# Performance work log

Measured on AMD Instinct MI355X. Metric: run time of the kernel, lower is better.

Reference implementation:

```python
import jax, jax.numpy as jnp
import numpy as np

N, E, G = 20000, 640000, 64
D_IN, H, C, D_OUT = 256, 4, 64, 32
HC = H * C


def gat_layer(x, W, a_src, a_dst, b, src, dst, n_nodes, heads, ch):
    # x: [N, F_in], W: [F_in, H*C]
    h = (x @ W).reshape(n_nodes, heads, ch)          # [N,H,C]
    es = jnp.einsum('nhc,hc->nh', h, a_src)          # [N,H]
    ed = jnp.einsum('nhc,hc->nh', h, a_dst)
    e = jax.nn.leaky_relu(es[src] + ed[dst], 0.2)    # [Etot,H]
    m = jax.ops.segment_max(e, dst, num_segments=n_nodes)
    m = jnp.where(jnp.isfinite(m), m, 0.0)
    ex = jnp.exp(e - m[dst])
    denom = jax.ops.segment_sum(ex, dst, num_segments=n_nodes)
    alpha = ex / jnp.maximum(denom[dst], 1e-16)      # softmax over in-edges per dst
    out = jax.ops.segment_sum(alpha[:, :, None] * h[src], dst, num_segments=n_nodes)
    return out.reshape(n_nodes, heads * ch) + b


def setup_inputs() -> dict:
    key = jax.random.key(0)
    ks = jax.random.split(key, 14)
    g1 = 1.0 / np.sqrt(D_IN)
    g2 = 1.0 / np.sqrt(HC)
    inp = {
        'x': jax.random.normal(ks[0], (N, D_IN), jnp.float32),
        'edge_index': jax.random.randint(ks[1], (2, E), 0, N, jnp.int64 if jax.config.jax_enable_x64 else jnp.int32),
        'batch': jnp.sort(jax.random.randint(ks[2], (N,), 0, G)),
        'W1': jax.random.normal(ks[3], (D_IN, HC), jnp.float32) * g1,
        'a_src1': jax.random.normal(ks[4], (H, C), jnp.float32) * g2,
        'a_dst1': jax.random.normal(ks[5], (H, C), jnp.float32) * g2,
        'b1': jnp.zeros((HC,), jnp.float32),
        'W2': jax.random.normal(ks[6], (HC, HC), jnp.float32) * g2,
        'a_src2': jax.random.normal(ks[7], (H, C), jnp.float32) * g2,
        'a_dst2': jax.random.normal(ks[8], (H, C), jnp.float32) * g2,
        'b2': jnp.zeros((HC,), jnp.float32),
        'Wp': jax.random.normal(ks[9], (HC, D_OUT), jnp.float32) * g2,
        'bp': jnp.zeros((D_OUT,), jnp.float32),
    }
    return inp


def reference(x, edge_index, batch, W1, a_src1, a_dst1, b1, W2, a_src2, a_dst2, b2, Wp, bp):
    # add self-loops (PyG GATConv default)
    loop = jnp.arange(N, dtype=edge_index.dtype)
    src = jnp.concatenate([edge_index[0], loop])
    dst = jnp.concatenate([edge_index[1], loop])
    x1 = jax.nn.relu(gat_layer(x, W1, a_src1, a_dst1, b1, src, dst, N, H, C))
    # dropout p=0.6 is identity in eval mode
    x2 = jax.nn.relu(gat_layer(x1, W2, a_src2, a_dst2, b2, src, dst, N, H, C))
    node_scores = x2 @ Wp + bp                        # [N, D_OUT]
    sums = jax.ops.segment_sum(node_scores, batch, num_segments=G)
    counts = jax.ops.segment_sum(jnp.ones((N,), node_scores.dtype), batch, num_segments=G)
    return sums / jnp.maximum(counts, 1.0)[:, None]   # [G, D_OUT]
```

## Files before the change

### kernel.cpp

```cpp
#include <hip/hip_runtime.h>
#include <hip/hip_bf16.h>
#include <cstdint>

#define NNODES 20000
#define NEDGES 640000
#define ETOT   (NEDGES + NNODES)
#define NGROUP 64
#define HC     256
#define DOUT   32

typedef short bf16x8 __attribute__((ext_vector_type(8)));
typedef short s16x4  __attribute__((ext_vector_type(4)));
typedef float f32x4  __attribute__((ext_vector_type(4)));
typedef float f32x2  __attribute__((ext_vector_type(2)));
typedef int   s32x4  __attribute__((ext_vector_type(4)));
typedef unsigned int u32x4 __attribute__((ext_vector_type(4)));

__device__ __forceinline__ float b2f(__hip_bfloat16 v) { return __bfloat162float(v); }
__device__ __forceinline__ float bs2f(short v) {
    union { unsigned int u; float f; } c; c.u = ((unsigned int)(unsigned short)v) << 16; return c.f;
}
__device__ __forceinline__ short f2bs(float v) {
    __hip_bfloat16 b = __float2bfloat16(v);
    union { __hip_bfloat16 b; short s; } u; u.b = b; return u.s;
}
__device__ __forceinline__ float ldf(const void* __restrict__ p, size_t i, int bf) {
    return bf ? __bfloat162float(((const __hip_bfloat16*)p)[i]) : ((const float*)p)[i];
}
__device__ __forceinline__ int ld_idx(const int* __restrict__ p, size_t i, int f64) {
    return f64 ? p[2 * i] : p[i];
}

__global__ void k_probe(const unsigned int* __restrict__ xw, const int* __restrict__ ei,
                        int* __restrict__ flag, int* __restrict__ deg) {
    int t = blockIdx.x * 256 + threadIdx.x;
    for (int i = t; i < NNODES; i += 256 * 32) deg[i] = 0;
    if (blockIdx.x == 0 && threadIdx.x < 64) {
        int l = threadIdx.x;
        int ones = 0, zeros = 0;
#pragma unroll
        for (int r = 0; r < 4; r++) {
            unsigned long long b1 = __ballot((xw[r * 64 + l] >> 14) & 1);
            unsigned long long b2 = __ballot(ei[2 * (r * 64 + l) + 1] == 0);
            ones  += __popcll(b1);
            zeros += __popcll(b2);
        }
        if (l == 0) { flag[1] = (ones < 64) ? 1 : 0; flag[0] = (zeros > 200) ? 1 : 0; }
    }
}

__global__ void k_hist(const int* __restrict__ ei, int* __restrict__ deg,
                       const int* __restrict__ flag) {
    int i = blockIdx.x * blockDim.x + threadIdx.x;
    if (i >= ETOT) return;
    int f = flag[0];
    int d = (i < NEDGES) ? ld_idx(ei, (size_t)NEDGES + i, f) : (i - NEDGES);
    atomicAdd(&deg[d], 1);
}

__global__ void k_scan(const int* __restrict__ deg, int* __restrict__ off, int* __restrict__ cur,
                       float* __restrict__ sx, int* __restrict__ cnt) {
    __shared__ int wsum[8];
    int t = threadIdx.x, lane = t & 63, wv = t >> 6;
    for (int i = t; i < NGROUP * HC; i += 512) sx[i] = 0.f;
    if (t < NGROUP) cnt[t] = 0;
    const int CH = ((NNODES + 511) / 512) * 64;
    int base = wv * CH;
    int s = 0;
    for (int i0 = 0; i0 < CH; i0 += 64) {
        int i = base + i0 + lane;
        s += (i < NNODES) ? deg[i] : 0;
    }
#pragma unroll
    for (int o = 1; o < 64; o <<= 1) s += __shfl_xor(s, o);
    if (lane == 0) wsum[wv] = s;
    __syncthreads();
    int run = 0;
    for (int i = 0; i < wv; i++) run += wsum[i];
    for (int i0 = 0; i0 < CH; i0 += 64) {
        int i = base + i0 + lane;
        int v = (i < NNODES) ? deg[i] : 0;
        int sc = v;
#pragma unroll
        for (int o = 1; o < 64; o <<= 1) {
            int u = __shfl_up(sc, o);
            if (lane >= o) sc += u;
        }
        if (i < NNODES) { int ex = run + sc - v; off[i] = ex; cur[i] = ex; }
        run += __shfl(sc, 63);
    }
    if (t == 0) off[NNODES] = ETOT;
}

__global__ void k_scatter(const int* __restrict__ ei, int* __restrict__ cur,
                          int* __restrict__ csr, const int* __restrict__ flag) {
    int i = blockIdx.x * blockDim.x + threadIdx.x;
    if (i >= ETOT) return;
    int f = flag[0];
    int s, d;
    if (i < NEDGES) { s = ld_idx(ei, i, f); d = ld_idx(ei, (size_t)NEDGES + i, f); }
    else            { s = d = i - NEDGES; }
    int pos = atomicAdd(&cur[d], 1);
    csr[pos] = s;
}

__global__ void k_wt(const void* __restrict__ W1, const void* __restrict__ W2,
                     __hip_bfloat16* __restrict__ Wt1, __hip_bfloat16* __restrict__ Wt2,
                     const int* __restrict__ flag) {
    int i = blockIdx.x * 256 + threadIdx.x;
    int which = i >> 16;
    int j = i & 65535;
    int k = j >> 8, n = j & 255;
    const void* W = which ? W2 : W1;
    __hip_bfloat16* Wt = which ? Wt2 : Wt1;
    Wt[(size_t)n * 256 + k] = __float2bfloat16(ldf(W, (size_t)k * 256 + n, flag[1]));
}

__global__ __launch_bounds__(256) void k_gemm(const void* __restrict__ A,
                                              const __hip_bfloat16* __restrict__ Bt,
                                              __hip_bfloat16* __restrict__ Hout,
                                              const void* __restrict__ a_src,
                                              const void* __restrict__ a_dst,
                                              float* __restrict__ es4, float* __restrict__ ed4,
                                              const int* __restrict__ flag, int force_bf) {
    int bf   = flag[1];
    int abf  = force_bf | bf;
    int w    = threadIdx.x >> 6;
    int lane = threadIdx.x & 63;
    int mr   = lane & 15;
    int quad = lane >> 4;
    int r0   = blockIdx.x * 16;
    if (r0 >= NNODES) return;
    f32x4 acc[4];
#pragma unroll
    for (int j = 0; j < 4; j++) acc[j] = (f32x4){0.f, 0.f, 0.f, 0.f};
    size_t rowoff = (size_t)(r0 + mr) * HC;
    const __hip_bfloat16* Btw = Bt + (size_t)w * 64 * HC;
    for (int kk = 0; kk < HC; kk += 32) {
        bf16x8 a;
        if (abf) {
            a = *reinterpret_cast<const bf16x8*>((const __hip_bfloat16*)A + rowoff + kk + quad * 8);
        } else {
            const float* af = (const float*)A + rowoff + kk + quad * 8;
            f32x4 lo = *reinterpret_cast<const f32x4*>(af);
            f32x4 hi = *reinterpret_cast<const f32x4*>(af + 4);
#pragma unroll
            for (int ii = 0; ii < 4; ii++) { a[ii] = f2bs(lo[ii]); a[ii + 4] = f2bs(hi[ii]); }
        }
#pragma unroll
        for (int j = 0; j < 4; j++) {
            bf16x8 b = *reinterpret_cast<const bf16x8*>(Btw + (size_t)(j * 16 + mr) * HC + kk + quad * 8);
            acc[j] = __builtin_amdgcn_mfma_f32_16x16x32_bf16(a, b, acc[j], 0, 0, 0);
        }
    }
#pragma unroll
    for (int j = 0; j < 4; j++)
#pragma unroll
        for (int r = 0; r < 4; r++)
            Hout[(size_t)(r0 + quad * 4 + r) * HC + w * 64 + j * 16 + mr] = __float2bfloat16(acc[j][r]);
    float ps[4] = {0.f, 0.f, 0.f, 0.f}, pd[4] = {0.f, 0.f, 0.f, 0.f};
#pragma unroll
    for (int j = 0; j < 4; j++) {
        float asv = ldf(a_src, (size_t)(w * 64 + j * 16 + mr), bf);
        float adv = ldf(a_dst, (size_t)(w * 64 + j * 16 + mr), bf);
#pragma unroll
        for (int r = 0; r < 4; r++) {
            ps[r] = fmaf(acc[j][r], asv, ps[r]);
            pd[r] = fmaf(acc[j][r], adv, pd[r]);
        }
    }
#pragma unroll
    for (int o = 1; o < 16; o <<= 1)
#pragma unroll
        for (int r = 0; r < 4; r++) {
            ps[r] += __shfl_xor(ps[r], o);
            pd[r] += __shfl_xor(pd[r], o);
        }
    if (mr == 0)
#pragma unroll
        for (int r = 0; r < 4; r++) {
            int row = r0 + quad * 4 + r;
            es4[(size_t)row * 4 + w] = ps[r];
            ed4[(size_t)row * 4 + w] = pd[r];
        }
}

__global__ __launch_bounds__(256) void k_score(const float* __restrict__ es4,
                                               const float* __restrict__ ed4,
                                               const int* __restrict__ off, const int* __restrict__ csr,
                                               float* __restrict__ alpha, float* __restrict__ rinv4) {
    int wv = threadIdx.x >> 6;
    int l  = threadIdx.x & 63;
    int n0 = blockIdx.x * 4 + wv;
    for (int n = n0; n < NNODES; n += 10000) {
        int base = off[n], deg = off[n + 1] - base;
        f32x4 edv = *reinterpret_cast<const f32x4*>(ed4 + (size_t)n * 4);
        f32x4 m = (f32x4){-INFINITY, -INFINITY, -INFINITY, -INFINITY};
        for (int c0 = 0; c0 < deg; c0 += 64) {
            int cn = min(deg - c0, 64);
            f32x4 ev;
            if (l < cn) {
                int s = csr[base + c0 + l];
                f32x4 e = *reinterpret_cast<const f32x4*>(es4 + (size_t)s * 4);
#pragma unroll
                for (int h = 0; h < 4; h++) {
                    float t = e[h] + edv[h];
                    ev[h] = (t > 0.f) ? t : 0.2f * t;
                }
            } else {
#pragma unroll
                for (int h = 0; h < 4; h++) ev[h] = -INFINITY;
            }
#pragma unroll
            for (int o = 32; o; o >>= 1)
#pragma unroll
                for (int h = 0; h < 4; h++) ev[h] = fmaxf(ev[h], __shfl_xor(ev[h], o));
#pragma unroll
            for (int h = 0; h < 4; h++) m[h] = fmaxf(m[h], ev[h]);
        }
        f32x4 ds = (f32x4){0.f, 0.f, 0.f, 0.f};
        for (int c0 = 0; c0 < deg; c0 += 64) {
            int cn = min(deg - c0, 64);
            f32x4 pv;
            if (l < cn) {
                int s = csr[base + c0 + l];
                f32x4 e = *reinterpret_cast<const f32x4*>(es4 + (size_t)s * 4);
#pragma unroll
                for (int h = 0; h < 4; h++) {
                    float t = e[h] + edv[h];
                    t = (t > 0.f) ? t : 0.2f * t;
                    pv[h] = __expf(t - m[h]);
                }
                *reinterpret_cast<f32x4*>(alpha + (size_t)(base + c0 + l) * 4) = pv;
            } else {
#pragma unroll
                for (int h = 0; h < 4; h++) pv[h] = 0.f;
            }
#pragma unroll
            for (int o = 32; o; o >>= 1)
#pragma unroll
                for (int h = 0; h < 4; h++) pv[h] += __shfl_xor(pv[h], o);
#pragma unroll
            for (int h = 0; h < 4; h++) ds[h] += pv[h];
        }
        if (l == 0) {
            f32x4 rv;
#pragma unroll
            for (int h = 0; h < 4; h++) rv[h] = 1.0f / fmaxf(ds[h], 1e-16f);
            *reinterpret_cast<f32x4*>(rinv4 + (size_t)n * 4) = rv;
        }
    }
}

__global__ __launch_bounds__(256) void k_agg(const __hip_bfloat16* __restrict__ Hb,
                                             const float* __restrict__ alpha,
                                             const float* __restrict__ rinv4,
                                             const void* __restrict__ bias,
                                             const int* __restrict__ off, const int* __restrict__ csr,
                                             const int* __restrict__ flag,
                                             __hip_bfloat16* __restrict__ out) {
    __shared__ float p_lds[4][4][64];
    __shared__ int   s_lds[4][64];
    int wv = threadIdx.x >> 6;
    int l  = threadIdx.x & 63;
    int half = l >> 5;
    int hl   = l & 31;
    int hd8  = hl >> 3;
    int bf = flag[1];
    int n0 = blockIdx.x * 4 + wv;
    for (int n = n0; n < NNODES; n += 10000) {
        int base = off[n], deg = off[n + 1] - base;
        f32x2 acc2[4];
#pragma unroll
        for (int d = 0; d < 4; d++) acc2[d] = (f32x2){0.f, 0.f};
        for (int c0 = 0; c0 < deg; c0 += 64) {
            int cn = min(deg - c0, 64);
            int s = 0;
            f32x4 a4 = (f32x4){0.f, 0.f, 0.f, 0.f};
            if (l < cn) {
                s  = csr[base + c0 + l];
                a4 = *reinterpret_cast<const f32x4*>(alpha + (size_t)(base + c0 + l) * 4);
            }
            s_lds[wv][l] = s;
#pragma unroll
            for (int h = 0; h < 4; h++) p_lds[wv][h][l] = a4[h];
            int jn = (cn + 15) & ~15;
            for (int j = 0; j < jn; j += 16) {
                int e0 = j + 8 * half;
                s32x4 sA = *reinterpret_cast<const s32x4*>(&s_lds[wv][e0]);
                s32x4 sB = *reinterpret_cast<const s32x4*>(&s_lds[wv][e0 + 4]);
                f32x4 pA = *reinterpret_cast<const f32x4*>(&p_lds[wv][hd8][e0]);
                f32x4 pB = *reinterpret_cast<const f32x4*>(&p_lds[wv][hd8][e0 + 4]);
                u32x4 hv[8];
#pragma unroll
                for (int i = 0; i < 8; i++) {
                    int sj = (i < 4) ? sA[i & 3] : sB[i & 3];
                    hv[i] = *reinterpret_cast<const u32x4*>(Hb + (size_t)sj * HC + hl * 8);
                }
#pragma unroll
                for (int i = 0; i < 8; i++) {
                    float p = (i < 4) ? pA[i & 3] : pB[i & 3];
#pragma unroll
                    for (int d = 0; d < 4; d++) {
                        unsigned int u = hv[i][d];
                        f32x2 h2;
                        h2.x = __uint_as_float(u << 16);
                        h2.y = __uint_as_float(u & 0xFFFF0000u);
                        acc2[d] += h2 * p;
                    }
                }
            }
        }
#pragma unroll
        for (int d = 0; d < 4; d++) {
            acc2[d].x += __shfl_xor(acc2[d].x, 32);
            acc2[d].y += __shfl_xor(acc2[d].y, 32);
        }
        f32x4 rv = *reinterpret_cast<const f32x4*>(rinv4 + (size_t)n * 4);
        float rinv = rv[hd8];
        if (half == 0) {
            bf16x8 ov;
#pragma unroll
            for (int d = 0; d < 4; d++) {
                float v0 = acc2[d].x * rinv + ldf(bias, (size_t)hl * 8 + 2 * d, bf);
                float v1 = acc2[d].y * rinv + ldf(bias, (size_t)hl * 8 + 2 * d + 1, bf);
                ov[2 * d]     = f2bs(fmaxf(v0, 0.f));
                ov[2 * d + 1] = f2bs(fmaxf(v1, 0.f));
            }
            *reinterpret_cast<bf16x8*>(out + (size_t)n * HC + hl * 8) = ov;
        }
    }
}

__global__ __launch_bounds__(256) void k_groupsum(const __hip_bfloat16* __restrict__ X2,
                                                  const int* __restrict__ batch,
                                                  float* __restrict__ sx, int* __restrict__ cnt,
                                                  const int* __restrict__ flag) {
    const int RPB = NNODES / 250;
    int b = blockIdx.x, f = flag[0];
    int sub = threadIdx.x >> 6, l = threadIdx.x & 63;
    int r = b * RPB + sub;
    f32x4 acc = (f32x4){0.f, 0.f, 0.f, 0.f};
    int curg = ld_idx(batch, r, f);
    int cacc = 0;
    for (int k = 0; k < RPB / 4; k++, r += 4) {
        int g = ld_idx(batch, r, f);
        if (g != curg) {
#pragma unroll
            for (int c = 0; c < 4; c++) atomicAdd(&sx[(size_t)curg * HC + l * 4 + c], acc[c]);
            if (l == 0) atomicAdd(&cnt[curg], cacc);
            acc = (f32x4){0.f, 0.f, 0.f, 0.f}; cacc = 0; curg = g;
        }
        s16x4 hv = *reinterpret_cast<const s16x4*>(X2 + (size_t)r * HC + l * 4);
#pragma unroll
        for (int c = 0; c < 4; c++) acc[c] += bs2f(hv[c]);
        cacc++;
    }
#pragma unroll
    for (int c = 0; c < 4; c++) atomicAdd(&sx[(size_t)curg * HC + l * 4 + c], acc[c]);
    if (l == 0) atomicAdd(&cnt[curg], cacc);
}

__global__ __launch_bounds__(256) void k_final(const float* __restrict__ sx,
                                               const void* __restrict__ Wp,
                                               const void* __restrict__ bp,
                                               const int* __restrict__ cnt,
                                               const int* __restrict__ flag,
                                               void* __restrict__ out) {
    __shared__ float red[8][32];
    int g = blockIdx.x, t = threadIdx.x;
    int c = t & 31, seg = t >> 5;
    int bf = flag[1];
    const float* sxg = sx + (size_t)g * HC;
    float a = 0.f;
#pragma unroll
    for (int k = 0; k < 32; k++) {
        int kk = seg * 32 + k;
        a = fmaf(sxg[kk], ldf(Wp, (size_t)kk * DOUT + c, bf), a);
    }
    red[seg][c] = a;
    __syncthreads();
    if (t < 32) {
        float s = 0.f;
#pragma unroll
        for (int i = 0; i < 8; i++) s += red[i][t];
        int ct = cnt[g];
        float v = (ct > 0) ? (s / ct + ldf(bp, (size_t)t, bf)) : 0.f;
        if (bf) ((__hip_bfloat16*)out)[g * DOUT + t] = __float2bfloat16(v);
        else    ((float*)out)[g * DOUT + t]          = v;
    }
}

extern "C" void kernel_launch(void* const* d_in, const int* in_sizes, int n_in,
                              void* d_out, int out_size, void* d_ws, size_t ws_size,
                              hipStream_t stream) {
    (void)in_sizes; (void)n_in; (void)out_size; (void)ws_size;
    const void* x   = d_in[0];
    const int*  ei  = (const int*)d_in[1];
    const int*  bat = (const int*)d_in[2];
    const void* W1  = d_in[3];
    const void* as1 = d_in[4];
    const void* ad1 = d_in[5];
    const void* b1  = d_in[6];
    const void* W2  = d_in[7];
    const void* as2 = d_in[8];
    const void* ad2 = d_in[9];
    const void* b2  = d_in[10];
    const void* Wp  = d_in[11];
    const void* bp  = d_in[12];

    char* ws = (char*)d_ws;
    size_t o = 0;
    auto alloc = [&](size_t bytes) -> char* {
        char* p = ws + o;
        o += (bytes + 255) & ~(size_t)255;
        return p;
    };
    __hip_bfloat16* hb  = (__hip_bfloat16*)alloc((size_t)NNODES * HC * 2);
    __hip_bfloat16* xb  = (__hip_bfloat16*)alloc((size_t)NNODES * HC * 2);
    __hip_bfloat16* xb2 = (__hip_bfloat16*)alloc((size_t)NNODES * HC * 2);
    __hip_bfloat16* Wt1 = (__hip_bfloat16*)alloc((size_t)HC * HC * 2);
    __hip_bfloat16* Wt2 = (__hip_bfloat16*)alloc((size_t)HC * HC * 2);
    float* es = (float*)alloc((size_t)NNODES * 4 * 4);
    float* ed = (float*)alloc((size_t)NNODES * 4 * 4);
    float* alpha = (float*)alloc((size_t)ETOT * 4 * 4);
    float* rinv  = (float*)alloc((size_t)NNODES * 4 * 4);
    int* deg  = (int*)alloc((size_t)NNODES * 4);
    int* cur  = (int*)alloc((size_t)NNODES * 4);
    int* off  = (int*)alloc((size_t)(NNODES + 1) * 4);
    int* csr  = (int*)alloc((size_t)ETOT * 4);
    float* sx = (float*)alloc((size_t)NGROUP * HC * 4);
    int* cnt  = (int*)alloc(256);
    int* flag = (int*)alloc(256);

    k_probe<<<32, 256, 0, stream>>>((const unsigned int*)x, ei, flag, deg);
    k_hist<<<(ETOT + 255) / 256, 256, 0, stream>>>(ei, deg, flag);
    k_scan<<<1, 512, 0, stream>>>(deg, off, cur, sx, cnt);
    k_scatter<<<(ETOT + 255) / 256, 256, 0, stream>>>(ei, cur, csr, flag);
    k_wt<<<512, 256, 0, stream>>>(W1, W2, Wt1, Wt2, flag);

    k_gemm<<<NNODES / 16, 256, 0, stream>>>(x, Wt1, hb, as1, ad1, es, ed, flag, 0);
    k_score<<<2500, 256, 0, stream>>>(es, ed, off, csr, alpha, rinv);
    k_agg<<<2500, 256, 0, stream>>>(hb, alpha, rinv, b1, off, csr, flag, xb);

    k_gemm<<<NNODES / 16, 256, 0, stream>>>(xb, Wt2, hb, as2, ad2, es, ed, flag, 1);
    k_score<<<2500, 256, 0, stream>>>(es, ed, off, csr, alpha, rinv);
    k_agg<<<2500, 256, 0, stream>>>(hb, alpha, rinv, b2, off, csr, flag, xb2);

    k_groupsum<<<250, 256, 0, stream>>>(xb2, bat, sx, cnt, flag);
    k_final<<<NGROUP, 256, 0, stream>>>(sx, Wp, bp, cnt, flag, d_out);
}
```

Before: 361.9 us.

## Fuse edge softmax into aggregation and build CSR with per-block LDS histograms

Two changes. First, the separate score kernel that wrote per-edge alpha and per-node inverse denominators is removed. The aggregation kernel now computes the leaky-relu scores inline and applies an online softmax, rescaling the running max, the denominator sum and the accumulators for each chunk of 64 edges. This drops the ETOT*16-byte alpha write/read and one launch per layer, at the cost of extra exp and shuffle work inside the aggregation loop. Second, CSR construction replaces global atomics with 128 blocks that each build a histogram in 80 KB of LDS (20000 ints), followed by column-sum, scan and per-block base-offset kernels and an LDS-atomic scatter. That is two more launches and a 10 MB histogram buffer in global memory, and it lowers occupancy because of the large LDS footprint.

After: 320.4 us. -11.5%, faster.

```diff
diff --git a/kernel.cpp b/kernel.cpp
--- a/kernel.cpp
+++ b/kernel.cpp
@@ -8,6 +8,8 @@
 #define NGROUP 64
 #define HC     256
 #define DOUT   32
+#define NB     128
+#define SL     ((ETOT + NB - 1) / NB)
 
 typedef short bf16x8 __attribute__((ext_vector_type(8)));
 typedef short s16x4  __attribute__((ext_vector_type(4)));
@@ -32,10 +34,8 @@
 }
 
 __global__ void k_probe(const unsigned int* __restrict__ xw, const int* __restrict__ ei,
-                        int* __restrict__ flag, int* __restrict__ deg) {
-    int t = blockIdx.x * 256 + threadIdx.x;
-    for (int i = t; i < NNODES; i += 256 * 32) deg[i] = 0;
-    if (blockIdx.x == 0 && threadIdx.x < 64) {
+                        int* __restrict__ flag) {
+    if (threadIdx.x < 64) {
         int l = threadIdx.x;
         int ones = 0, zeros = 0;
 #pragma unroll
@@ -49,16 +49,34 @@
     }
 }
 
-__global__ void k_hist(const int* __restrict__ ei, int* __restrict__ deg,
-                       const int* __restrict__ flag) {
-    int i = blockIdx.x * blockDim.x + threadIdx.x;
-    if (i >= ETOT) return;
-    int f = flag[0];
-    int d = (i < NEDGES) ? ld_idx(ei, (size_t)NEDGES + i, f) : (i - NEDGES);
-    atomicAdd(&deg[d], 1);
-}
-
-__global__ void k_scan(const int* __restrict__ deg, int* __restrict__ off, int* __restrict__ cur,
+__global__ __launch_bounds__(256) void k_lhist(const int* __restrict__ ei,
+                                               int* __restrict__ H,
+                                               const int* __restrict__ flag) {
+    __shared__ int hl[NNODES];
+    int t = threadIdx.x, b = blockIdx.x, f = flag[0];
+    for (int i = t; i < NNODES; i += 256) hl[i] = 0;
+    __syncthreads();
+    int s0 = b * SL, s1 = min(s0 + SL, ETOT);
+    for (int i = s0 + t; i < s1; i += 256) {
+        int d = (i < NEDGES) ? ld_idx(ei, (size_t)NEDGES + i, f) : (i - NEDGES);
+        atomicAdd(&hl[d], 1);
+    }
+    __syncthreads();
+    int* Hb = H + (size_t)b * NNODES;
+    for (int i = t; i < NNODES; i += 256) Hb[i] = hl[i];
+}
+
+__global__ __launch_bounds__(256) void k_colsum(const int* __restrict__ H,
+                                                int* __restrict__ deg) {
+    int n = blockIdx.x * 256 + threadIdx.x;
+    if (n >= NNODES) return;
+    int s = 0;
+#pragma unroll 4
+    for (int b = 0; b < NB; b++) s += H[(size_t)b * NNODES + n];
+    deg[n] = s;
+}
+
+__global__ void k_scan(const int* __restrict__ deg, int* __restrict__ off,
                        float* __restrict__ sx, int* __restrict__ cnt) {
     __shared__ int wsum[8];
     int t = threadIdx.x, lane = t & 63, wv = t >> 6;
@@ -86,22 +104,43 @@
             int u = __shfl_up(sc, o);
             if (lane >= o) sc += u;
         }
-        if (i < NNODES) { int ex = run + sc - v; off[i] = ex; cur[i] = ex; }
+        if (i < NNODES) off[i] = run + sc - v;
         run += __shfl(sc, 63);
     }
     if (t == 0) off[NNODES] = ETOT;
 }
 
-__global__ void k_scatter(const int* __restrict__ ei, int* __restrict__ cur,
-                          int* __restrict__ csr, const int* __restrict__ flag) {
-    int i = blockIdx.x * blockDim.x + threadIdx.x;
-    if (i >= ETOT) return;
-    int f = flag[0];
-    int s, d;
-    if (i < NEDGES) { s = ld_idx(ei, i, f); d = ld_idx(ei, (size_t)NEDGES + i, f); }
-    else            { s = d = i - NEDGES; }
-    int pos = atomicAdd(&cur[d], 1);
-    csr[pos] = s;
+__global__ __launch_bounds__(256) void k_base(int* __restrict__ H,
+                                              const int* __restrict__ off) {
+    int n = blockIdx.x * 256 + threadIdx.x;
+    if (n >= NNODES) return;
+    int run = off[n];
+#pragma unroll 4
+    for (int b = 0; b < NB; b++) {
+        size_t idx = (size_t)b * NNODES + n;
+        int t = H[idx];
+        H[idx] = run;
+        run += t;
+    }
+}
+
+__global__ __launch_bounds__(256) void k_scatter2(const int* __restrict__ ei,
+                                                  const int* __restrict__ H,
+                                                  int* __restrict__ csr,
+                                                  const int* __restrict__ flag) {
+    __shared__ int base_l[NNODES];
+    int t = threadIdx.x, b = blockIdx.x, f = flag[0];
+    const int* Hb = H + (size_t)b * NNODES;
+    for (int i = t; i < NNODES; i += 256) base_l[i] = Hb[i];
+    __syncthreads();
+    int s0 = b * SL, s1 = min(s0 + SL, ETOT);
+    for (int i = s0 + t; i < s1; i += 256) {
+        int s, d;
+        if (i < NEDGES) { s = ld_idx(ei, i, f); d = ld_idx(ei, (size_t)NEDGES + i, f); }
+        else            { s = d = i - NEDGES; }
+        int pos = atomicAdd(&base_l[d], 1);
+        csr[pos] = s;
+    }
 }
 
 __global__ void k_wt(const void* __restrict__ W1, const void* __restrict__ W2,
@@ -185,76 +224,8 @@
         }
 }
 
-__global__ __launch_bounds__(256) void k_score(const float* __restrict__ es4,
-                                               const float* __restrict__ ed4,
-                                               const int* __restrict__ off, const int* __restrict__ csr,
-                                               float* __restrict__ alpha, float* __restrict__ rinv4) {
-    int wv = threadIdx.x >> 6;
-    int l  = threadIdx.x & 63;
-    int n0 = blockIdx.x * 4 + wv;
-    for (int n = n0; n < NNODES; n += 10000) {
-        int base = off[n], deg = off[n + 1] - base;
-        f32x4 edv = *reinterpret_cast<const f32x4*>(ed4 + (size_t)n * 4);
-        f32x4 m = (f32x4){-INFINITY, -INFINITY, -INFINITY, -INFINITY};
-        for (int c0 = 0; c0 < deg; c0 += 64) {
-            int cn = min(deg - c0, 64);
-            f32x4 ev;
-            if (l < cn) {
-                int s = csr[base + c0 + l];
-                f32x4 e = *reinterpret_cast<const f32x4*>(es4 + (size_t)s * 4);
-#pragma unroll
-                for (int h = 0; h < 4; h++) {
-                    float t = e[h] + edv[h];
-                    ev[h] = (t > 0.f) ? t : 0.2f * t;
-                }
-            } else {
-#pragma unroll
-                for (int h = 0; h < 4; h++) ev[h] = -INFINITY;
-            }
-#pragma unroll
-            for (int o = 32; o; o >>= 1)
-#pragma unroll
-                for (int h = 0; h < 4; h++) ev[h] = fmaxf(ev[h], __shfl_xor(ev[h], o));
-#pragma unroll
-            for (int h = 0; h < 4; h++) m[h] = fmaxf(m[h], ev[h]);
-        }
-        f32x4 ds = (f32x4){0.f, 0.f, 0.f, 0.f};
-        for (int c0 = 0; c0 < deg; c0 += 64) {
-            int cn = min(deg - c0, 64);
-            f32x4 pv;
-            if (l < cn) {
-                int s = csr[base + c0 + l];
-                f32x4 e = *reinterpret_cast<const f32x4*>(es4 + (size_t)s * 4);
-#pragma unroll
-                for (int h = 0; h < 4; h++) {
-                    float t = e[h] + edv[h];
-                    t = (t > 0.f) ? t : 0.2f * t;
-                    pv[h] = __expf(t - m[h]);
-                }
-                *reinterpret_cast<f32x4*>(alpha + (size_t)(base + c0 + l) * 4) = pv;
-            } else {
-#pragma unroll
-                for (int h = 0; h < 4; h++) pv[h] = 0.f;
-            }
-#pragma unroll
-            for (int o = 32; o; o >>= 1)
-#pragma unroll
-                for (int h = 0; h < 4; h++) pv[h] += __shfl_xor(pv[h], o);
-#pragma unroll
-            for (int h = 0; h < 4; h++) ds[h] += pv[h];
-        }
-        if (l == 0) {
-            f32x4 rv;
-#pragma unroll
-            for (int h = 0; h < 4; h++) rv[h] = 1.0f / fmaxf(ds[h], 1e-16f);
-            *reinterpret_cast<f32x4*>(rinv4 + (size_t)n * 4) = rv;
-        }
-    }
-}
-
 __global__ __launch_bounds__(256) void k_agg(const __hip_bfloat16* __restrict__ Hb,
-                                             const float* __restrict__ alpha,
-                                             const float* __restrict__ rinv4,
+                                             const float* __restrict__ es4, const float* __restrict__ ed4,
                                              const void* __restrict__ bias,
                                              const int* __restrict__ off, const int* __restrict__ csr,
                                              const int* __restrict__ flag,
@@ -270,20 +241,55 @@
     int n0 = blockIdx.x * 4 + wv;
     for (int n = n0; n < NNODES; n += 10000) {
         int base = off[n], deg = off[n + 1] - base;
+        f32x4 edv = *reinterpret_cast<const f32x4*>(ed4 + (size_t)n * 4);
+        f32x4 m    = (f32x4){-INFINITY, -INFINITY, -INFINITY, -INFINITY};
+        f32x4 dsum = (f32x4){0.f, 0.f, 0.f, 0.f};
         f32x2 acc2[4];
 #pragma unroll
         for (int d = 0; d < 4; d++) acc2[d] = (f32x2){0.f, 0.f};
         for (int c0 = 0; c0 < deg; c0 += 64) {
             int cn = min(deg - c0, 64);
             int s = 0;
-            f32x4 a4 = (f32x4){0.f, 0.f, 0.f, 0.f};
+            f32x4 ev;
             if (l < cn) {
-                s  = csr[base + c0 + l];
-                a4 = *reinterpret_cast<const f32x4*>(alpha + (size_t)(base + c0 + l) * 4);
+                s = csr[base + c0 + l];
+                f32x4 e = *reinterpret_cast<const f32x4*>(es4 + (size_t)s * 4);
+#pragma unroll
+                for (int h = 0; h < 4; h++) {
+                    float t = e[h] + edv[h];
+                    ev[h] = (t > 0.f) ? t : 0.2f * t;
+                }
+            } else {
+#pragma unroll
+                for (int h = 0; h < 4; h++) ev[h] = -INFINITY;
             }
             s_lds[wv][l] = s;
-#pragma unroll
-            for (int h = 0; h < 4; h++) p_lds[wv][h][l] = a4[h];
+            f32x4 mc = ev;
+#pragma unroll
+            for (int o = 32; o; o >>= 1)
+#pragma unroll
+                for (int h = 0; h < 4; h++) mc[h] = fmaxf(mc[h], __shfl_xor(mc[h], o));
+            f32x4 al, pv;
+#pragma unroll
+            for (int h = 0; h < 4; h++) {
+                float nm = fmaxf(m[h], mc[h]);
+                al[h] = __expf(m[h] - nm);
+                m[h]  = nm;
+            }
+#pragma unroll
+            for (int h = 0; h < 4; h++) pv[h] = (l < cn) ? __expf(ev[h] - m[h]) : 0.f;
+            f32x4 sc = pv;
+#pragma unroll
+            for (int o = 32; o; o >>= 1)
+#pragma unroll
+                for (int h = 0; h < 4; h++) sc[h] += __shfl_xor(sc[h], o);
+#pragma unroll
+            for (int h = 0; h < 4; h++) dsum[h] = dsum[h] * al[h] + sc[h];
+            float a8 = al[hd8];
+#pragma unroll
+            for (int d = 0; d < 4; d++) acc2[d] *= a8;
+#pragma unroll
+            for (int h = 0; h < 4; h++) p_lds[wv][h][l] = pv[h];
             int jn = (cn + 15) & ~15;
             for (int j = 0; j < jn; j += 16) {
                 int e0 = j + 8 * half;
@@ -316,8 +322,7 @@
             acc2[d].x += __shfl_xor(acc2[d].x, 32);
             acc2[d].y += __shfl_xor(acc2[d].y, 32);
         }
-        f32x4 rv = *reinterpret_cast<const f32x4*>(rinv4 + (size_t)n * 4);
-        float rinv = rv[hd8];
+        float rinv = 1.0f / fmaxf(dsum[hd8], 1e-16f);
         if (half == 0) {
             bf16x8 ov;
 #pragma unroll
@@ -423,29 +428,27 @@
     __hip_bfloat16* Wt2 = (__hip_bfloat16*)alloc((size_t)HC * HC * 2);
     float* es = (float*)alloc((size_t)NNODES * 4 * 4);
     float* ed = (float*)alloc((size_t)NNODES * 4 * 4);
-    float* alpha = (float*)alloc((size_t)ETOT * 4 * 4);
-    float* rinv  = (float*)alloc((size_t)NNODES * 4 * 4);
+    int* H    = (int*)alloc((size_t)NB * NNODES * 4);
     int* deg  = (int*)alloc((size_t)NNODES * 4);
-    int* cur  = (int*)alloc((size_t)NNODES * 4);
     int* off  = (int*)alloc((size_t)(NNODES + 1) * 4);
     int* csr  = (int*)alloc((size_t)ETOT * 4);
     float* sx = (float*)alloc((size_t)NGROUP * HC * 4);
     int* cnt  = (int*)alloc(256);
     int* flag = (int*)alloc(256);
 
-    k_probe<<<32, 256, 0, stream>>>((const unsigned int*)x, ei, flag, deg);
-    k_hist<<<(ETOT + 255) / 256, 256, 0, stream>>>(ei, deg, flag);
-    k_scan<<<1, 512, 0, stream>>>(deg, off, cur, sx, cnt);
-    k_scatter<<<(ETOT + 255) / 256, 256, 0, stream>>>(ei, cur, csr, flag);
+    k_probe<<<1, 256, 0, stream>>>((const unsigned int*)x, ei, flag);
+    k_lhist<<<NB, 256, 0, stream>>>(ei, H, flag);
+    k_colsum<<<(NNODES + 255) / 256, 256, 0, stream>>>(H, deg);
+    k_scan<<<1, 512, 0, stream>>>(deg, off, sx, cnt);
+    k_base<<<(NNODES + 255) / 256, 256, 0, stream>>>(H, off);
+    k_scatter2<<<NB, 256, 0, stream>>>(ei, H, csr, flag);
     k_wt<<<512, 256, 0, stream>>>(W1, W2, Wt1, Wt2, flag);
 
     k_gemm<<<NNODES / 16, 256, 0, stream>>>(x, Wt1, hb, as1, ad1, es, ed, flag, 0);
-    k_score<<<2500, 256, 0, stream>>>(es, ed, off, csr, alpha, rinv);
-    k_agg<<<2500, 256, 0, stream>>>(hb, alpha, rinv, b1, off, csr, flag, xb);
+    k_agg<<<2500, 256, 0, stream>>>(hb, es, ed, b1, off, csr, flag, xb);
 
     k_gemm<<<NNODES / 16, 256, 0, stream>>>(xb, Wt2, hb, as2, ad2, es, ed, flag, 1);
-    k_score<<<2500, 256, 0, stream>>>(es, ed, off, csr, alpha, rinv);
-    k_agg<<<2500, 256, 0, stream>>>(hb, alpha, rinv, b2, off, csr, flag, xb2);
+    k_agg<<<2500, 256, 0, stream>>>(hb, es, ed, b2, off, csr, flag, xb2);
 
     k_groupsum<<<250, 256, 0, stream>>>(xb2, bat, sx, cnt, flag);
     k_final<<<NGROUP, 256, 0, stream>>>(sx, Wp, bp, cnt, flag, d_out);
```
